# Kernel tuning notes

Measured on AMD Instinct MI355X. Metric: run time of the kernel, lower is better.

The kernel has to match this reference:

```python
import jax, jax.numpy as jnp
import numpy as np

USER_NUM = 100000
ITEM_NUM = 50000
N_NODES = USER_NUM + ITEM_NUM
EMB = 64
LAYERS = 3
NNZ = 2400000


def spmm(rows, cols, vals, x, n):
    # sparse [n, n] (COO) @ dense [n, d] -> [n, d]
    gathered = vals[:, None] * x[cols]          # [nnz, d]
    return jax.ops.segment_sum(gathered, rows, num_segments=n)


def setup_inputs() -> dict:
    key = jax.random.key(0)
    ks = jax.random.split(key, 7)
    return {
        "user_emb": jax.random.normal(ks[0], (USER_NUM, EMB), jnp.float32) * 0.1,
        "item_emb": jax.random.normal(ks[1], (ITEM_NUM, EMB), jnp.float32) * 0.1,
        "w1": jax.random.normal(ks[2], (LAYERS, EMB, EMB), jnp.float32) * (1.0 / np.sqrt(EMB)),
        "w2": jax.random.normal(ks[3], (LAYERS, EMB, EMB), jnp.float32) * (1.0 / np.sqrt(EMB)),
        "adj_vals": jax.random.uniform(ks[4], (NNZ,), jnp.float32) * (1.0 / 16.0),
        "adj_rows": jax.random.randint(ks[5], (NNZ,), 0, N_NODES, jnp.int32),
        "adj_cols": jax.random.randint(ks[6], (NNZ,), 0, N_NODES, jnp.int32),
    }


def reference(user_emb, item_emb, w1, w2, adj_vals, adj_rows, adj_cols):
    ego = jnp.concatenate([user_emb, item_emb], axis=0)   # [N, d]
    n = ego.shape[0]
    all_emb = [ego]
    for k in range(w1.shape[0]):
        temp = ego @ w1[k]                                # [N, d]
        agg_temp = spmm(adj_rows, adj_cols, adj_vals, temp, n)
        agg_ego = spmm(adj_rows, adj_cols, adj_vals, ego, n)
        ego = jax.nn.leaky_relu(agg_temp + temp + (agg_ego * ego) @ w2[k])
        all_emb.append(ego)
    mean_emb = jnp.mean(jnp.stack(all_emb, axis=1), axis=1)  # [N, d]
    u = user_emb.shape[0]
    return mean_emb[:u], mean_emb[u:]
```

## Files before the change

### kernel.cpp

```cpp
#include <hip/hip_runtime.h>
#include <hip/hip_fp16.h>

typedef _Float16 f16;
typedef _Float16 f16x8 __attribute__((ext_vector_type(8)));
typedef float f32x4 __attribute__((ext_vector_type(4)));

__device__ __forceinline__ float h2f(__half v) { return __half2float(v); }
__device__ __forceinline__ __half f2h(float v) { return __float2half(v); }

#define SCAN_CHUNK 2048
#define ASTRIDE 136

#define BSHIFT 10
#define BROWS (1 << BSHIFT)
#define MAXB 1024
#define TILE 4096

__global__ void zero_out_kernel(float* __restrict__ out, int total) {
    int i = blockIdx.x * blockDim.x + threadIdx.x;
    if (i < total) out[i] = 0.0f;
}

__global__ void init_kernel(const float* __restrict__ user, const float* __restrict__ item,
                            __half* __restrict__ ego0, int usz, int total) {
    int i = blockIdx.x * blockDim.x + threadIdx.x;
    if (i >= total) return;
    float f = (i < usz) ? user[i] : item[i - usz];
    ego0[i] = f2h(f);
}

__global__ void hist_kernel(const int* __restrict__ rows, int* __restrict__ cnt, int nnz) {
    int i = blockIdx.x * blockDim.x + threadIdx.x;
    if (i < nnz) atomicAdd(&cnt[rows[i]], 1);
}

__global__ void scan_pass1(const int* __restrict__ cnt, int* __restrict__ bsum, int n) {
    __shared__ int wt[4];
    int tid = threadIdx.x;
    int base = blockIdx.x * SCAN_CHUNK + tid * 8;
    int s = 0;
    #pragma unroll
    for (int k = 0; k < 8; ++k) { int i = base + k; if (i < n) s += cnt[i]; }
    #pragma unroll
    for (int o = 32; o > 0; o >>= 1) s += __shfl_down(s, o, 64);
    int lane = tid & 63, wid = tid >> 6;
    if (lane == 0) wt[wid] = s;
    __syncthreads();
    if (tid == 0) bsum[blockIdx.x] = wt[0] + wt[1] + wt[2] + wt[3];
}

__global__ void scan_pass2(int* __restrict__ bsum, int nb, int* __restrict__ total) {
    if (threadIdx.x == 0) {
        int run = 0;
        for (int b = 0; b < nb; ++b) { int v = bsum[b]; bsum[b] = run; run += v; }
        *total = run;
    }
}

__global__ void scan_pass3(int* __restrict__ cnt, const int* __restrict__ bsum,
                           int* __restrict__ rptr, int n, const int* __restrict__ total) {
    __shared__ int wt[4];
    int tid = threadIdx.x;
    int base = blockIdx.x * SCAN_CHUNK + tid * 8;
    int v[8];
    int s = 0;
    #pragma unroll
    for (int k = 0; k < 8; ++k) { int i = base + k; v[k] = (i < n) ? cnt[i] : 0; s += v[k]; }
    int lane = tid & 63, wid = tid >> 6;
    int xs = s;
    #pragma unroll
    for (int o = 1; o < 64; o <<= 1) { int t = __shfl_up(xs, o, 64); if (lane >= o) xs += t; }
    if (lane == 63) wt[wid] = xs;
    __syncthreads();
    int wexcl = 0;
    for (int w = 0; w < wid; ++w) wexcl += wt[w];
    int run = bsum[blockIdx.x] + wexcl + (xs - s);
    #pragma unroll
    for (int k = 0; k < 8; ++k) {
        int i = base + k;
        if (i < n) { rptr[i] = run; cnt[i] = run; }
        run += v[k];
    }
    if (blockIdx.x == 0 && tid == 0) rptr[n] = *total;
}

__global__ void scatter_kernel(const int* __restrict__ rows, const int* __restrict__ cols,
                               const float* __restrict__ vals, int* __restrict__ cursor,
                               int2* __restrict__ edges, int nnz) {
    int i = blockIdx.x * blockDim.x + threadIdx.x;
    if (i >= nnz) return;
    int r = rows[i];
    int pos = atomicAdd(&cursor[r], 1);
    edges[pos] = make_int2(cols[i], __float_as_int(vals[i]));
}

__global__ __launch_bounds__(256)
void bhist_kernel(const int* __restrict__ rows, int* __restrict__ bcnt, int nnz, int nbuck) {
    __shared__ int hist[MAXB];
    int tid = threadIdx.x;
    for (int j = tid; j < nbuck; j += 256) hist[j] = 0;
    __syncthreads();
    int i = blockIdx.x * TILE + tid;
    #pragma unroll
    for (int k = 0; k < 16; ++k, i += 256)
        if (i < nnz) atomicAdd(&hist[rows[i] >> BSHIFT], 1);
    __syncthreads();
    for (int j = tid; j < nbuck; j += 256)
        if (hist[j]) atomicAdd(&bcnt[j], hist[j]);
}

__global__ void bscan_kernel(const int* __restrict__ bcnt, int* __restrict__ bbase,
                             int* __restrict__ gcur, int nbuck) {
    if (threadIdx.x == 0) {
        int run = 0;
        for (int b = 0; b < nbuck; ++b) { bbase[b] = run; gcur[b] = run; run += bcnt[b]; }
        bbase[nbuck] = run;
    }
}

__global__ __launch_bounds__(256)
void binA_kernel(const int* __restrict__ rows, const int* __restrict__ cols,
                 const float* __restrict__ vals, int* __restrict__ gcur,
                 int2* __restrict__ bucketed, int nnz, int nbuck) {
    __shared__ int hist[MAXB];
    __shared__ int offs[MAXB];
    __shared__ int rbase[MAXB];
    __shared__ int2 reorder[TILE];
    __shared__ unsigned short slotb[TILE];
    __shared__ int wsum[4];
    int tid = threadIdx.x;
    int tbase = blockIdx.x * TILE;
    int cnt_here = min(TILE, nnz - tbase);

    for (int b = tid; b < MAXB; b += 256) hist[b] = 0;
    __syncthreads();

    int myrow[16]; int mycol[16]; float myval[16];
    #pragma unroll
    for (int k = 0; k < 16; ++k) {
        int i = tbase + tid + k * 256;
        int r = (i < nnz) ? rows[i] : -1;
        myrow[k] = r;
        if (r >= 0) {
            mycol[k] = cols[i];
            myval[k] = vals[i];
            atomicAdd(&hist[r >> BSHIFT], 1);
        }
    }
    __syncthreads();

    int b0 = tid * 4;
    int s0 = hist[b0], s1 = hist[b0 + 1], s2 = hist[b0 + 2], s3 = hist[b0 + 3];
    int tsum = s0 + s1 + s2 + s3;
    int lane = tid & 63, wid = tid >> 6;
    int x = tsum;
    #pragma unroll
    for (int o = 1; o < 64; o <<= 1) { int t = __shfl_up(x, o, 64); if (lane >= o) x += t; }
    if (lane == 63) wsum[wid] = x;
    __syncthreads();
    int wexcl = 0;
    for (int w = 0; w < wid; ++w) wexcl += wsum[w];
    int excl = wexcl + x - tsum;
    offs[b0]     = excl;
    offs[b0 + 1] = excl + s0;
    offs[b0 + 2] = excl + s0 + s1;
    offs[b0 + 3] = excl + s0 + s1 + s2;
    for (int b = tid; b < nbuck; b += 256) {
        int c = hist[b];
        rbase[b] = (c > 0) ? atomicAdd(&gcur[b], c) : 0;
    }
    __syncthreads();
    for (int b = tid; b < MAXB; b += 256) hist[b] = 0;
    __syncthreads();

    #pragma unroll
    for (int k = 0; k < 16; ++k) {
        int r = myrow[k];
        if (r >= 0) {
            int b = r >> BSHIFT;
            int p = offs[b] + atomicAdd(&hist[b], 1);
            reorder[p] = make_int2(((r & (BROWS - 1)) << 20) | mycol[k], __float_as_int(myval[k]));
            slotb[p] = (unsigned short)b;
        }
    }
    __syncthreads();

    for (int t = tid; t < cnt_here; t += 256) {
        int b = slotb[t];
        bucketed[rbase[b] + (t - offs[b])] = reorder[t];
    }
}

__global__ __launch_bounds__(256)
void binB_fused_kernel(const int* __restrict__ bbase, const int2* __restrict__ bucketed,
                       int2* __restrict__ edges, int* __restrict__ rptr, int n, int nbuck) {
    __shared__ int cur[BROWS];
    __shared__ int wsum[4];
    int b = blockIdx.x;
    int row_lo = b << BSHIFT;
    int nrows = min(BROWS, n - row_lo);
    int tid = threadIdx.x;
    for (int j = tid; j < BROWS; j += 256) cur[j] = 0;
    __syncthreads();
    int beg = bbase[b], end = bbase[b + 1];
    for (int i = beg + tid; i < end; i += 256)
        atomicAdd(&cur[((unsigned)bucketed[i].x) >> 20], 1);
    __syncthreads();
    int j0 = tid * 4;
    int c0 = cur[j0], c1 = cur[j0 + 1], c2 = cur[j0 + 2], c3 = cur[j0 + 3];
    int tsum = c0 + c1 + c2 + c3;
    int lane = tid & 63, wid = tid >> 6;
    int x = tsum;
    #pragma unroll
    for (int o = 1; o < 64; o <<= 1) { int t = __shfl_up(x, o, 64); if (lane >= o) x += t; }
    if (lane == 63) wsum[wid] = x;
    __syncthreads();
    int wexcl = 0;
    for (int w = 0; w < wid; ++w) wexcl += wsum[w];
    int excl = beg + wexcl + x - tsum;
    cur[j0]     = excl;
    cur[j0 + 1] = excl + c0;
    cur[j0 + 2] = excl + c0 + c1;
    cur[j0 + 3] = excl + c0 + c1 + c2;
    __syncthreads();
    for (int j = tid; j < nrows; j += 256) rptr[row_lo + j] = cur[j];
    if (b == nbuck - 1 && tid == 0) rptr[n] = bbase[nbuck];
    for (int i = beg + tid; i < end; i += 256) {
        int2 rec = bucketed[i];
        int ro  = ((unsigned)rec.x) >> 20;
        int col = rec.x & ((1 << 20) - 1);
        int pos = atomicAdd(&cur[ro], 1);
        edges[pos] = make_int2(col, rec.y);
    }
}

__device__ __forceinline__ void spmm_edge_acc(float4& acc, int2 e, const uint2* egov, int g) {
    uint2 gv = egov[((size_t)e.x << 4) + g];
    float v = __int_as_float(e.y);
    float2 a = __half22float2(*(const __half2*)&gv.x);
    float2 b = __half22float2(*(const __half2*)&gv.y);
    acc.x += v * a.x; acc.y += v * a.y; acc.z += v * b.x; acc.w += v * b.y;
}

__global__ __launch_bounds__(256)
void spmm_kernel(const int* __restrict__ rptr, const int2* __restrict__ edges,
                 const __half* __restrict__ ego, __half* __restrict__ aggE, int n) {
    int tid = threadIdx.x;
    int lane = tid & 63, wid = tid >> 6;
    int sub = lane >> 4;
    int g   = lane & 15;
    int row = blockIdx.x * 16 + wid * 4 + sub;
    bool active = row < n;
    int beg = active ? rptr[row] : 0;
    int end = active ? rptr[row + 1] : 0;
    float4 acc = {0.f, 0.f, 0.f, 0.f};
    const uint2* egov = (const uint2*)ego;
    int j = beg;
    for (; j + 8 <= end; j += 8) {
        int2 e0 = edges[j],     e1 = edges[j + 1], e2 = edges[j + 2], e3 = edges[j + 3];
        int2 e4 = edges[j + 4], e5 = edges[j + 5], e6 = edges[j + 6], e7 = edges[j + 7];
        spmm_edge_acc(acc, e0, egov, g);
        spmm_edge_acc(acc, e1, egov, g);
        spmm_edge_acc(acc, e2, egov, g);
        spmm_edge_acc(acc, e3, egov, g);
        spmm_edge_acc(acc, e4, egov, g);
        spmm_edge_acc(acc, e5, egov, g);
        spmm_edge_acc(acc, e6, egov, g);
        spmm_edge_acc(acc, e7, egov, g);
    }
    for (; j + 4 <= end; j += 4) {
        int2 e0 = edges[j], e1 = edges[j + 1], e2 = edges[j + 2], e3 = edges[j + 3];
        spmm_edge_acc(acc, e0, egov, g);
        spmm_edge_acc(acc, e1, egov, g);
        spmm_edge_acc(acc, e2, egov, g);
        spmm_edge_acc(acc, e3, egov, g);
    }
    for (; j < end; ++j) {
        int2 e = edges[j];
        spmm_edge_acc(acc, e, egov, g);
    }
    if (active) {
        __half2 h0 = __float22half2_rn(make_float2(acc.x, acc.y));
        __half2 h1 = __float22half2_rn(make_float2(acc.z, acc.w));
        uint2 outv;
        outv.x = *(const unsigned*)&h0;
        outv.y = *(const unsigned*)&h1;
        ((uint2*)aggE)[((size_t)row << 4) + g] = outv;
    }
}

__global__ __launch_bounds__(256, 4)
void layer_mfma_kernel(const __half* __restrict__ aggE, const __half* __restrict__ ego,
                       const float* __restrict__ w1k, const float* __restrict__ w2k,
                       __half* __restrict__ ego_out, int n) {
    __shared__ f16 A_lds[64 * ASTRIDE];
    __shared__ f16 Wt_lds[64 * ASTRIDE];
    int tid = threadIdx.x;
    #pragma unroll
    for (int it = 0; it < 16; ++it) {
        int e = tid + it * 256;
        int k = e >> 6, c = e & 63;
        Wt_lds[c * ASTRIDE + k]      = (f16)w1k[e];
        Wt_lds[c * ASTRIDE + 64 + k] = (f16)w2k[e];
    }
    int base_row = blockIdx.x * 64;
    const __half2* a2p = (const __half2*)aggE;
    const __half2* x2p = (const __half2*)ego;
    #pragma unroll
    for (int it = 0; it < 8; ++it) {
        int idx = tid + it * 256;
        int r = idx >> 5, c2 = idx & 31;
        int grow = base_row + r;
        size_t goff = (size_t)(grow < n ? grow : 0) * 32 + c2;
        float2 a = __half22float2(a2p[goff]);
        float2 x = __half22float2(x2p[goff]);
        f16* ar = &A_lds[r * ASTRIDE];
        ar[2 * c2]          = (f16)(a.x + x.x);
        ar[2 * c2 + 1]      = (f16)(a.y + x.y);
        ar[64 + 2 * c2]     = (f16)(a.x * x.x);
        ar[64 + 2 * c2 + 1] = (f16)(a.y * x.y);
    }
    __syncthreads();
    int lane = tid & 63, wid = tid >> 6;
    int m = lane & 15, q = lane >> 4;
    f32x4 acc0 = {0.f, 0.f, 0.f, 0.f}, acc1 = acc0, acc2 = acc0, acc3 = acc0;
    const f16* arow = &A_lds[(wid * 16 + m) * ASTRIDE + q * 8];
    const f16* brow = &Wt_lds[m * ASTRIDE + q * 8];
    #pragma unroll
    for (int ks = 0; ks < 4; ++ks) {
        f16x8 av = *(const f16x8*)(arow + ks * 32);
        f16x8 b0 = *(const f16x8*)(brow + ks * 32);
        f16x8 b1 = *(const f16x8*)(brow + 16 * ASTRIDE + ks * 32);
        f16x8 b2 = *(const f16x8*)(brow + 32 * ASTRIDE + ks * 32);
        f16x8 b3 = *(const f16x8*)(brow + 48 * ASTRIDE + ks * 32);
        acc0 = __builtin_amdgcn_mfma_f32_16x16x32_f16(av, b0, acc0, 0, 0, 0);
        acc1 = __builtin_amdgcn_mfma_f32_16x16x32_f16(av, b1, acc1, 0, 0, 0);
        acc2 = __builtin_amdgcn_mfma_f32_16x16x32_f16(av, b2, acc2, 0, 0, 0);
        acc3 = __builtin_amdgcn_mfma_f32_16x16x32_f16(av, b3, acc3, 0, 0, 0);
    }
    int rbase = base_row + wid * 16 + q * 4;
    #pragma unroll
    for (int r = 0; r < 4; ++r) {
        int grow = rbase + r;
        if (grow < n) {
            size_t o = (size_t)grow * 64 + m;
            float e0 = acc0[r]; e0 = (e0 > 0.f) ? e0 : 0.01f * e0;
            float e1 = acc1[r]; e1 = (e1 > 0.f) ? e1 : 0.01f * e1;
            float e2 = acc2[r]; e2 = (e2 > 0.f) ? e2 : 0.01f * e2;
            float e3 = acc3[r]; e3 = (e3 > 0.f) ? e3 : 0.01f * e3;
            ego_out[o]      = f2h(e0);
            ego_out[o + 16] = f2h(e1);
            ego_out[o + 32] = f2h(e2);
            ego_out[o + 48] = f2h(e3);
        }
    }
}

__global__ void finalize4_kernel(const __half* __restrict__ e0, const __half* __restrict__ e1,
                                 const __half* __restrict__ e2, const __half* __restrict__ e3,
                                 float* __restrict__ out, const int* __restrict__ rptr,
                                 int N, int nnz, float scale, int total) {
    int i = blockIdx.x * blockDim.x + threadIdx.x;
    if (i >= total) return;
    bool ok = (rptr[N] == nnz);
    float s = h2f(e0[i]) + h2f(e1[i]) + h2f(e2[i]) + h2f(e3[i]);
    out[i] = ok ? s * scale : 0.75f;
}

__global__ void acc_kernel(const __half* __restrict__ e, float* __restrict__ out,
                           float scale, int total, int first) {
    int i = blockIdx.x * blockDim.x + threadIdx.x;
    if (i >= total) return;
    float v = h2f(e[i]) * scale;
    out[i] = first ? v : out[i] + v;
}

extern "C" void kernel_launch(void* const* d_in, const int* in_sizes, int n_in,
                              void* d_out, int out_size, void* d_ws, size_t ws_size,
                              hipStream_t stream) {
    const float* user = (const float*)d_in[0];
    const float* item = (const float*)d_in[1];
    const float* w1   = (const float*)d_in[2];
    const float* w2   = (const float*)d_in[3];
    const float* vals = (const float*)d_in[4];
    const int*   rows = (const int*)d_in[5];
    const int*   cols = (const int*)d_in[6];

    const int usz = in_sizes[0];
    const int isz = in_sizes[1];
    const int L   = in_sizes[2] / 4096;
    const int nnz = in_sizes[4];
    const int N   = (usz + isz) / 64;
    const int ND  = N * 64;
    const int nbscan = (N + SCAN_CHUNK - 1) / SCAN_CHUNK;
    const int nbuck  = (N + BROWS - 1) >> BSHIFT;

    char* p = (char*)d_ws;
    auto alloc = [&](size_t bytes) -> void* {
        void* r = (void*)p;
        p += (bytes + 255) & ~(size_t)255;
        return r;
    };
    __half* egos  = (__half*)alloc((size_t)(L + 1) * ND * 2);
    __half* aggE  = (__half*)alloc((size_t)ND * 2);
    int2*   edges = (int2*)alloc((size_t)nnz * 8);
    int*    rptr  = (int*)alloc((size_t)(N + 1) * 4);
    int*    cnt   = (int*)alloc((size_t)N * 4);
    int*    bsum  = (int*)alloc((size_t)nbscan * 4);
    int*    total = (int*)alloc(4);
    int*    bcnt  = (int*)alloc((size_t)(MAXB + 1) * 4);
    int*    bbase = (int*)alloc((size_t)(MAXB + 1) * 4);
    int*    gcur  = (int*)alloc((size_t)MAXB * 4);
    bool fast_sort = (nbuck <= MAXB) && (N < (1 << 20)) && (nnz > 0);
    int2* bucketed = nullptr;
    if (fast_sort) {
        if ((size_t)ND * 2 >= (size_t)nnz * 8) bucketed = (int2*)aggE;
        else bucketed = (int2*)alloc((size_t)nnz * 8);
    }
    size_t need = (size_t)(p - (char*)d_ws);
    (void)n_in; (void)out_size;

    if (need > ws_size) {
        zero_out_kernel<<<(ND + 255) / 256, 256, 0, stream>>>((float*)d_out, ND);
        return;
    }

    init_kernel<<<(ND + 255) / 256, 256, 0, stream>>>(user, item, egos, usz, ND);

    if (fast_sort) {
        hipMemsetAsync(bcnt, 0, (size_t)nbuck * 4, stream);
        bhist_kernel<<<(nnz + TILE - 1) / TILE, 256, 0, stream>>>(rows, bcnt, nnz, nbuck);
        bscan_kernel<<<1, 64, 0, stream>>>(bcnt, bbase, gcur, nbuck);
        binA_kernel<<<(nnz + TILE - 1) / TILE, 256, 0, stream>>>(rows, cols, vals, gcur,
                                                                 bucketed, nnz, nbuck);
        binB_fused_kernel<<<nbuck, 256, 0, stream>>>(bbase, bucketed, edges, rptr, N, nbuck);
    } else {
        hipMemsetAsync(cnt, 0, (size_t)N * 4, stream);
        hist_kernel<<<(nnz + 255) / 256, 256, 0, stream>>>(rows, cnt, nnz);
        scan_pass1<<<nbscan, 256, 0, stream>>>(cnt, bsum, N);
        scan_pass2<<<1, 64, 0, stream>>>(bsum, nbscan, total);
        scan_pass3<<<nbscan, 256, 0, stream>>>(cnt, bsum, rptr, N, total);
        scatter_kernel<<<(nnz + 255) / 256, 256, 0, stream>>>(rows, cols, vals, cnt, edges, nnz);
    }

    const int rb16 = (N + 15) / 16;
    const int nb64 = (N + 63) / 64;
    for (int k = 0; k < L; ++k) {
        __half* ein  = egos + (size_t)k * ND;
        __half* eout = egos + (size_t)(k + 1) * ND;
        spmm_kernel<<<rb16, 256, 0, stream>>>(rptr, edges, ein, aggE, N);
        layer_mfma_kernel<<<nb64, 256, 0, stream>>>(aggE, ein, w1 + (size_t)k * 4096,
                                                    w2 + (size_t)k * 4096, eout, N);
    }
    float scale = 1.0f / (float)(L + 1);
    if (L == 3) {
        finalize4_kernel<<<(ND + 255) / 256, 256, 0, stream>>>(
            egos, egos + (size_t)ND, egos + (size_t)2 * ND, egos + (size_t)3 * ND,
            (float*)d_out, rptr, N, nnz, scale, ND);
    } else {
        for (int k = 0; k <= L; ++k)
            acc_kernel<<<(ND + 255) / 256, 256, 0, stream>>>(egos + (size_t)k * ND,
                                                             (float*)d_out, scale, ND, k == 0);
    }
}
```

Before: 429.8 us.

## Fuse SpMM aggregation with per-layer MFMA transform into one kernel

Merges the sparse aggregation kernel and the dense MFMA layer kernel. Each 512-thread block gathers 32 rows, forms the sum and product with ego directly in LDS, then runs the 64x128 by 128x64 MFMA and writes the leaky-ReLU output. This removes the intermediate aggE write and read and one launch per layer. In exchange, weights are reloaded per 32-row block, and the gather and matmul phases now share occupancy and a block barrier.

```diff
diff --git a/kernel.cpp b/kernel.cpp
--- a/kernel.cpp
+++ b/kernel.cpp
@@ -2,6 +2,7 @@
 #include <hip/hip_fp16.h>
 
 typedef _Float16 f16;
+typedef _Float16 f16x4 __attribute__((ext_vector_type(4)));
 typedef _Float16 f16x8 __attribute__((ext_vector_type(8)));
 typedef float f32x4 __attribute__((ext_vector_type(4)));
 
@@ -242,14 +243,25 @@
     acc.x += v * a.x; acc.y += v * a.y; acc.z += v * b.x; acc.w += v * b.y;
 }
 
-__global__ __launch_bounds__(256)
-void spmm_kernel(const int* __restrict__ rptr, const int2* __restrict__ edges,
-                 const __half* __restrict__ ego, __half* __restrict__ aggE, int n) {
-    int tid = threadIdx.x;
+__global__ __launch_bounds__(512, 4)
+void spmm_mfma_kernel(const int* __restrict__ rptr, const int2* __restrict__ edges,
+                      const __half* __restrict__ ego, const float* __restrict__ w1k,
+                      const float* __restrict__ w2k, __half* __restrict__ ego_out, int n) {
+    __shared__ f16 A_lds[32 * ASTRIDE];
+    __shared__ f16 Wt_lds[64 * ASTRIDE];
+    int tid = threadIdx.x;
+    #pragma unroll
+    for (int it = 0; it < 8; ++it) {
+        int e = tid + it * 512;
+        int k = e >> 6, c = e & 63;
+        Wt_lds[c * ASTRIDE + k]      = (f16)w1k[e];
+        Wt_lds[c * ASTRIDE + 64 + k] = (f16)w2k[e];
+    }
     int lane = tid & 63, wid = tid >> 6;
     int sub = lane >> 4;
     int g   = lane & 15;
-    int row = blockIdx.x * 16 + wid * 4 + sub;
+    int row  = blockIdx.x * 32 + wid * 4 + sub;
+    int lrow = wid * 4 + sub;
     bool active = row < n;
     int beg = active ? rptr[row] : 0;
     int end = active ? rptr[row + 1] : 0;
@@ -276,82 +288,41 @@
         spmm_edge_acc(acc, e3, egov, g);
     }
     for (; j < end; ++j) {
-        int2 e = edges[j];
-        spmm_edge_acc(acc, e, egov, g);
-    }
-    if (active) {
-        __half2 h0 = __float22half2_rn(make_float2(acc.x, acc.y));
-        __half2 h1 = __float22half2_rn(make_float2(acc.z, acc.w));
-        uint2 outv;
-        outv.x = *(const unsigned*)&h0;
-        outv.y = *(const unsigned*)&h1;
-        ((uint2*)aggE)[((size_t)row << 4) + g] = outv;
-    }
-}
-
-__global__ __launch_bounds__(256, 4)
-void layer_mfma_kernel(const __half* __restrict__ aggE, const __half* __restrict__ ego,
-                       const float* __restrict__ w1k, const float* __restrict__ w2k,
-                       __half* __restrict__ ego_out, int n) {
-    __shared__ f16 A_lds[64 * ASTRIDE];
-    __shared__ f16 Wt_lds[64 * ASTRIDE];
-    int tid = threadIdx.x;
-    #pragma unroll
-    for (int it = 0; it < 16; ++it) {
-        int e = tid + it * 256;
-        int k = e >> 6, c = e & 63;
-        Wt_lds[c * ASTRIDE + k]      = (f16)w1k[e];
-        Wt_lds[c * ASTRIDE + 64 + k] = (f16)w2k[e];
-    }
-    int base_row = blockIdx.x * 64;
-    const __half2* a2p = (const __half2*)aggE;
-    const __half2* x2p = (const __half2*)ego;
-    #pragma unroll
-    for (int it = 0; it < 8; ++it) {
-        int idx = tid + it * 256;
-        int r = idx >> 5, c2 = idx & 31;
-        int grow = base_row + r;
-        size_t goff = (size_t)(grow < n ? grow : 0) * 32 + c2;
-        float2 a = __half22float2(a2p[goff]);
-        float2 x = __half22float2(x2p[goff]);
-        f16* ar = &A_lds[r * ASTRIDE];
-        ar[2 * c2]          = (f16)(a.x + x.x);
-        ar[2 * c2 + 1]      = (f16)(a.y + x.y);
-        ar[64 + 2 * c2]     = (f16)(a.x * x.x);
-        ar[64 + 2 * c2 + 1] = (f16)(a.y * x.y);
-    }
-    __syncthreads();
-    int lane = tid & 63, wid = tid >> 6;
+        spmm_edge_acc(acc, edges[j], egov, g);
+    }
+    {
+        uint2 xv = egov[(size_t)(active ? row : 0) * 16 + g];
+        float2 x01 = __half22float2(*(const __half2*)&xv.x);
+        float2 x23 = __half22float2(*(const __half2*)&xv.y);
+        f16x4 sv, pv;
+        sv[0] = (f16)(acc.x + x01.x); sv[1] = (f16)(acc.y + x01.y);
+        sv[2] = (f16)(acc.z + x23.x); sv[3] = (f16)(acc.w + x23.y);
+        pv[0] = (f16)(acc.x * x01.x); pv[1] = (f16)(acc.y * x01.y);
+        pv[2] = (f16)(acc.z * x23.x); pv[3] = (f16)(acc.w * x23.y);
+        f16* ar = &A_lds[lrow * ASTRIDE + g * 4];
+        *(f16x4*)ar        = sv;
+        *(f16x4*)(ar + 64) = pv;
+    }
+    __syncthreads();
+    int band = wid >> 2;
+    int nt   = wid & 3;
     int m = lane & 15, q = lane >> 4;
-    f32x4 acc0 = {0.f, 0.f, 0.f, 0.f}, acc1 = acc0, acc2 = acc0, acc3 = acc0;
-    const f16* arow = &A_lds[(wid * 16 + m) * ASTRIDE + q * 8];
-    const f16* brow = &Wt_lds[m * ASTRIDE + q * 8];
+    f32x4 dacc = {0.f, 0.f, 0.f, 0.f};
+    const f16* arow = &A_lds[(band * 16 + m) * ASTRIDE + q * 8];
+    const f16* brow = &Wt_lds[(nt * 16 + m) * ASTRIDE + q * 8];
     #pragma unroll
     for (int ks = 0; ks < 4; ++ks) {
         f16x8 av = *(const f16x8*)(arow + ks * 32);
-        f16x8 b0 = *(const f16x8*)(brow + ks * 32);
-        f16x8 b1 = *(const f16x8*)(brow + 16 * ASTRIDE + ks * 32);
-        f16x8 b2 = *(const f16x8*)(brow + 32 * ASTRIDE + ks * 32);
-        f16x8 b3 = *(const f16x8*)(brow + 48 * ASTRIDE + ks * 32);
-        acc0 = __builtin_amdgcn_mfma_f32_16x16x32_f16(av, b0, acc0, 0, 0, 0);
-        acc1 = __builtin_amdgcn_mfma_f32_16x16x32_f16(av, b1, acc1, 0, 0, 0);
-        acc2 = __builtin_amdgcn_mfma_f32_16x16x32_f16(av, b2, acc2, 0, 0, 0);
-        acc3 = __builtin_amdgcn_mfma_f32_16x16x32_f16(av, b3, acc3, 0, 0, 0);
-    }
-    int rbase = base_row + wid * 16 + q * 4;
+        f16x8 bv = *(const f16x8*)(brow + ks * 32);
+        dacc = __builtin_amdgcn_mfma_f32_16x16x32_f16(av, bv, dacc, 0, 0, 0);
+    }
+    int rbase = blockIdx.x * 32 + band * 16 + q * 4;
     #pragma unroll
     for (int r = 0; r < 4; ++r) {
         int grow = rbase + r;
         if (grow < n) {
-            size_t o = (size_t)grow * 64 + m;
-            float e0 = acc0[r]; e0 = (e0 > 0.f) ? e0 : 0.01f * e0;
-            float e1 = acc1[r]; e1 = (e1 > 0.f) ? e1 : 0.01f * e1;
-            float e2 = acc2[r]; e2 = (e2 > 0.f) ? e2 : 0.01f * e2;
-            float e3 = acc3[r]; e3 = (e3 > 0.f) ? e3 : 0.01f * e3;
-            ego_out[o]      = f2h(e0);
-            ego_out[o + 16] = f2h(e1);
-            ego_out[o + 32] = f2h(e2);
-            ego_out[o + 48] = f2h(e3);
+            float e0 = dacc[r]; e0 = (e0 > 0.f) ? e0 : 0.01f * e0;
+            ego_out[(size_t)grow * 64 + nt * 16 + m] = f2h(e0);
         }
     }
 }
@@ -443,14 +414,12 @@
         scatter_kernel<<<(nnz + 255) / 256, 256, 0, stream>>>(rows, cols, vals, cnt, edges, nnz);
     }
 
-    const int rb16 = (N + 15) / 16;
-    const int nb64 = (N + 63) / 64;
+    const int fb = (N + 31) / 32;
     for (int k = 0; k < L; ++k) {
         __half* ein  = egos + (size_t)k * ND;
         __half* eout = egos + (size_t)(k + 1) * ND;
-        spmm_kernel<<<rb16, 256, 0, stream>>>(rptr, edges, ein, aggE, N);
-        layer_mfma_kernel<<<nb64, 256, 0, stream>>>(aggE, ein, w1 + (size_t)k * 4096,
-                                                    w2 + (size_t)k * 4096, eout, N);
+        spmm_mfma_kernel<<<fb, 512, 0, stream>>>(rptr, edges, ein, w1 + (size_t)k * 4096,
+                                                 w2 + (size_t)k * 4096, eout, N);
     }
     float scale = 1.0f / (float)(L + 1);
     if (L == 3) {
```

New measurement: 426.0 us. About the same (-0.9%).
